# Optimization experiments

Hardware: AMD Instinct MI355X
Metric: run time of the kernel (lower is better)

## Reference

```python
import jax, jax.numpy as jnp
import numpy as np

NEG_INF = -1e30  # stand-in for -inf, safe under fp16/bf16 softmax masking via where below


def setup_inputs() -> dict:
    key = jax.random.key(0)
    ks = jax.random.split(key, 6)
    B, S, D, E = 4, 4096, 2048, 16
    x = jax.random.normal(ks[0], (B, S, D), dtype=jnp.float32)
    noise = jax.random.normal(ks[1], (B, S, E), dtype=jnp.float32)
    scale = 1.0 / np.sqrt(D)
    W_fc = jax.random.normal(ks[2], (E, D), dtype=jnp.float32) * scale
    b_fc = jnp.zeros((E,), dtype=jnp.float32)
    W_noisy = jax.random.normal(ks[3], (E, D), dtype=jnp.float32) * scale
    b_noisy = jnp.zeros((E,), dtype=jnp.float32)
    return {"x": x, "noise": noise, "W_fc": W_fc, "b_fc": b_fc,
            "W_noisy": W_noisy, "b_noisy": b_noisy}


def reference(x, noise, W_fc, b_fc, W_noisy, b_noisy):
    top_k = 2
    n_expert = W_fc.shape[0]
    # dual linear: [B,S,D] @ [D,E] -> [B,S,E]
    logits = jnp.einsum("bsd,ed->bse", x, W_fc) + b_fc
    noise_logits = jnp.einsum("bsd,ed->bse", x, W_noisy) + b_noisy
    noisy_logits = logits + noise * jax.nn.softplus(noise_logits)
    top_k_logits, ids = jax.lax.top_k(noisy_logits, top_k)  # [B,S,k]
    # scatter top-k values into a -inf-filled tensor == mask non-topk with -inf
    sel = jnp.any(jax.nn.one_hot(ids, n_expert, dtype=jnp.bool_), axis=-2)  # [B,S,E]
    sparse_logits = jnp.where(sel, noisy_logits, -jnp.inf)
    router_output = jax.nn.softmax(sparse_logits, axis=-1)
    return (router_output, ids)
```

## Files before the change

kernel.cpp:

```cpp
#include <hip/hip_runtime.h>
#include <hip/hip_bf16.h>

#define NROWS 16384
#define KD    2048
#define NE    16
#define ROWS_PER_BLK 64
#define KH    1024
#define TPH   16


__device__ __forceinline__ void gload_lds16(const float* g, float* l) {
    __builtin_amdgcn_global_load_lds(
        (const __attribute__((address_space(1))) void*)g,
        (__attribute__((address_space(3))) void*)l,
        16, 0, 0);
}

__global__ __launch_bounds__(512)
void noisy_router_kernel(const float* __restrict__ x,
                         const float* __restrict__ noise,
                         const float* __restrict__ Wfc,
                         const float* __restrict__ bfc,
                         const float* __restrict__ Wns,
                         const float* __restrict__ bns,
                         float* __restrict__ out)
{
    __shared__ float lds[32 * KH + ROWS_PER_BLK * 33];

    const int tid  = threadIdx.x;
    const int lane = tid & 63;
    const int w    = tid >> 6;
    const int eq   = w & 3;
    const int rh   = w >> 2;
    const int seg  = lane & 7;
    const int rgrp = lane >> 3;

    const int rowbase = blockIdx.x * ROWS_PER_BLK + rh * 32 + rgrp * 4;

    const int wrb  = tid >> 8;
    const int scol = (tid & 255) * 4;

    const float* xb = x + (size_t)rowbase * KD + seg * 8;

    float accA[4][4], accB[4][4];
    #pragma unroll
    for (int j = 0; j < 4; ++j)
        #pragma unroll
        for (int e = 0; e < 4; ++e) { accA[j][e] = 0.f; accB[j][e] = 0.f; }

    #pragma unroll 1
    for (int h = 0; h < 2; ++h) {
        const int kbase = h * KH;
        __syncthreads();
        {
            const float* srcF = Wfc + (size_t)wrb * KD + kbase + scol;
            const float* srcN = Wns + (size_t)wrb * KD + kbase + scol;
            #pragma unroll
            for (int i = 0; i < 8; ++i)
                gload_lds16(srcF + (size_t)(2 * i) * KD, lds + i * 2048 + tid * 4);
            #pragma unroll
            for (int i = 0; i < 8; ++i)
                gload_lds16(srcN + (size_t)(2 * i) * KD, lds + (8 + i) * 2048 + tid * 4);
        }
        __syncthreads();

        const float* wp0 = lds + (eq * 4) * KH + seg * 8;
        const float* wp1 = lds + (16 + eq * 4) * KH + seg * 8;
        const float* xh  = xb + kbase;

        #pragma unroll 2
        for (int t = 0; t < TPH; ++t) {
            float4 xv[4][2];
            #pragma unroll
            for (int j = 0; j < 4; ++j) {
                xv[j][0] = *(const float4*)(xh + (size_t)j * KD + t * 64);
                xv[j][1] = *(const float4*)(xh + (size_t)j * KD + t * 64 + 4);
            }
            #pragma unroll
            for (int e = 0; e < 4; ++e) {
                const float4 a0 = *(const float4*)(wp0 + e * KH + t * 64);
                const float4 a1 = *(const float4*)(wp0 + e * KH + t * 64 + 4);
                const float4 b0 = *(const float4*)(wp1 + e * KH + t * 64);
                const float4 b1 = *(const float4*)(wp1 + e * KH + t * 64 + 4);
                #pragma unroll
                for (int j = 0; j < 4; ++j) {
                    const float4 x0 = xv[j][0], x1 = xv[j][1];
                    float sA = accA[j][e], sB = accB[j][e];
                    sA = fmaf(x0.x, a0.x, sA); sA = fmaf(x0.y, a0.y, sA);
                    sA = fmaf(x0.z, a0.z, sA); sA = fmaf(x0.w, a0.w, sA);
                    sA = fmaf(x1.x, a1.x, sA); sA = fmaf(x1.y, a1.y, sA);
                    sA = fmaf(x1.z, a1.z, sA); sA = fmaf(x1.w, a1.w, sA);
                    sB = fmaf(x0.x, b0.x, sB); sB = fmaf(x0.y, b0.y, sB);
                    sB = fmaf(x0.z, b0.z, sB); sB = fmaf(x0.w, b0.w, sB);
                    sB = fmaf(x1.x, b1.x, sB); sB = fmaf(x1.y, b1.y, sB);
                    sB = fmaf(x1.z, b1.z, sB); sB = fmaf(x1.w, b1.w, sB);
                    accA[j][e] = sA; accB[j][e] = sB;
                }
            }
        }
    }

    #pragma unroll
    for (int j = 0; j < 4; ++j)
        #pragma unroll
        for (int e = 0; e < 4; ++e) {
            float a = accA[j][e], b = accB[j][e];
            a += __shfl_xor(a, 1); a += __shfl_xor(a, 2); a += __shfl_xor(a, 4);
            b += __shfl_xor(b, 1); b += __shfl_xor(b, 2); b += __shfl_xor(b, 4);
            accA[j][e] = a; accB[j][e] = b;
        }

    __syncthreads();
    float* const slab = lds + 32 * KH;

    if (seg == 0) {
        #pragma unroll
        for (int j = 0; j < 4; ++j) {
            float* dst = slab + (rh * 32 + rgrp * 4 + j) * 33 + eq * 4;
            #pragma unroll
            for (int e = 0; e < 4; ++e) { dst[e] = accA[j][e]; dst[16 + e] = accB[j][e]; }
        }
    }
    __syncthreads();

    if (tid < ROWS_PER_BLK) {
        const int r = tid;
        const float* rowp = slab + r * 33;
        const size_t grow = (size_t)blockIdx.x * ROWS_PER_BLK + r;
        const float* nzp = noise + grow * NE;

        float m1 = -1e30f, m2 = -1e30f;
        int i1 = 0, i2 = 0;
        #pragma unroll
        for (int j = 0; j < NE; ++j) {
            const float z  = rowp[16 + j] + bns[j];
            const float sp = fmaxf(z, 0.f) + log1pf(expf(-fabsf(z)));
            const float v  = fmaf(nzp[j], sp, rowp[j] + bfc[j]);
            if (v > m1)      { m2 = m1; i2 = i1; m1 = v; i1 = j; }
            else if (v > m2) { m2 = v;  i2 = j; }
        }
        const float e2  = expf(m2 - m1);
        const float inv = 1.f / (1.f + e2);

        float* po = out + grow * NE;
        #pragma unroll
        for (int j = 0; j < NE; ++j) {
            po[j] = (j == i1) ? inv : ((j == i2) ? e2 * inv : 0.f);
        }
        float* pi = out + (size_t)NROWS * NE + grow * 2;
        pi[0] = (float)i1;
        pi[1] = (float)i2;
    }
}

extern "C" void kernel_launch(void* const* d_in, const int* in_sizes, int n_in,
                              void* d_out, int out_size, void* d_ws, size_t ws_size,
                              hipStream_t stream)
{
    const float* x     = (const float*)d_in[0];
    const float* noise = (const float*)d_in[1];
    const float* Wfc   = (const float*)d_in[2];
    const float* bfc   = (const float*)d_in[3];
    const float* Wns   = (const float*)d_in[4];
    const float* bns   = (const float*)d_in[5];
    float* out = (float*)d_out;

    noisy_router_kernel<<<NROWS / ROWS_PER_BLK, 512, 0, stream>>>(
        x, noise, Wfc, bfc, Wns, bns, out);
}
```

Before: 48.66 us.

## Halve rows per block and split K across wave groups with LDS reduction

Reduces rows per block from 64 to 32, doubling the grid to 512 blocks. The two wave groups now split each K chunk rather than owning separate row halves. Weights are staged in four 512-wide phases instead of two 1024-wide ones, and the partial sums are combined through an LDS reduction. This aims to spread work across more CUs and cut LDS footprint for better occupancy, at the cost of twice the total weight staging traffic and an extra barrier and reduction step.

```diff
diff --git a/kernel.cpp b/kernel.cpp
--- a/kernel.cpp
+++ b/kernel.cpp
@@ -4,9 +4,10 @@
 #define NROWS 16384
 #define KD    2048
 #define NE    16
-#define ROWS_PER_BLK 64
-#define KH    1024
-#define TPH   16
+#define ROWS_PER_BLK 32
+#define KQ    512
+#define NPH   4
+#define TPP   8
 
 
 __device__ __forceinline__ void gload_lds16(const float* g, float* l) {
@@ -25,20 +26,20 @@
                          const float* __restrict__ bns,
                          float* __restrict__ out)
 {
-    __shared__ float lds[32 * KH + ROWS_PER_BLK * 33];
+    __shared__ float lds[32 * KQ + 2 * 32 * 33];
 
     const int tid  = threadIdx.x;
     const int lane = tid & 63;
     const int w    = tid >> 6;
     const int eq   = w & 3;
-    const int rh   = w >> 2;
+    const int kg   = w >> 2;
     const int seg  = lane & 7;
     const int rgrp = lane >> 3;
 
-    const int rowbase = blockIdx.x * ROWS_PER_BLK + rh * 32 + rgrp * 4;
+    const int rowbase = blockIdx.x * ROWS_PER_BLK + rgrp * 4;
 
-    const int wrb  = tid >> 8;
-    const int scol = (tid & 255) * 4;
+    const int swr  = tid >> 7;
+    const int scol = (tid & 127) * 4;
 
     const float* xb = x + (size_t)rowbase * KD + seg * 8;
 
@@ -49,27 +50,28 @@
         for (int e = 0; e < 4; ++e) { accA[j][e] = 0.f; accB[j][e] = 0.f; }
 
     #pragma unroll 1
-    for (int h = 0; h < 2; ++h) {
-        const int kbase = h * KH;
+    for (int p = 0; p < NPH; ++p) {
+        const int kbase = p * KQ;
         __syncthreads();
         {
-            const float* srcF = Wfc + (size_t)wrb * KD + kbase + scol;
-            const float* srcN = Wns + (size_t)wrb * KD + kbase + scol;
             #pragma unroll
-            for (int i = 0; i < 8; ++i)
-                gload_lds16(srcF + (size_t)(2 * i) * KD, lds + i * 2048 + tid * 4);
-            #pragma unroll
-            for (int i = 0; i < 8; ++i)
-                gload_lds16(srcN + (size_t)(2 * i) * KD, lds + (8 + i) * 2048 + tid * 4);
+            for (int i = 0; i < 8; ++i) {
+                const int wr = 4 * i + swr;
+                const float* gsrc = (wr < 16 ? Wfc + (size_t)wr * KD
+                                             : Wns + (size_t)(wr - 16) * KD)
+                                    + kbase + scol;
+                gload_lds16(gsrc, lds + i * 2048 + tid * 4);
+            }
         }
         __syncthreads();
 
-        const float* wp0 = lds + (eq * 4) * KH + seg * 8;
-        const float* wp1 = lds + (16 + eq * 4) * KH + seg * 8;
+        const float* wp0 = lds + (eq * 4) * KQ + seg * 8;
+        const float* wp1 = lds + (16 + eq * 4) * KQ + seg * 8;
         const float* xh  = xb + kbase;
 
         #pragma unroll 2
-        for (int t = 0; t < TPH; ++t) {
+        for (int c = 0; c < 4; ++c) {
+            const int t = kg * 4 + c;
             float4 xv[4][2];
             #pragma unroll
             for (int j = 0; j < 4; ++j) {
@@ -78,10 +80,10 @@
             }
             #pragma unroll
             for (int e = 0; e < 4; ++e) {
-                const float4 a0 = *(const float4*)(wp0 + e * KH + t * 64);
-                const float4 a1 = *(const float4*)(wp0 + e * KH + t * 64 + 4);
-                const float4 b0 = *(const float4*)(wp1 + e * KH + t * 64);
-                const float4 b1 = *(const float4*)(wp1 + e * KH + t * 64 + 4);
+                const float4 a0 = *(const float4*)(wp0 + e * KQ + t * 64);
+                const float4 a1 = *(const float4*)(wp0 + e * KQ + t * 64 + 4);
+                const float4 b0 = *(const float4*)(wp1 + e * KQ + t * 64);
+                const float4 b1 = *(const float4*)(wp1 + e * KQ + t * 64 + 4);
                 #pragma unroll
                 for (int j = 0; j < 4; ++j) {
                     const float4 x0 = xv[j][0], x1 = xv[j][1];
@@ -111,15 +113,24 @@
         }
 
     __syncthreads();
-    float* const slab = lds + 32 * KH;
+    float* const slab = lds + 32 * KQ;
 
     if (seg == 0) {
         #pragma unroll
         for (int j = 0; j < 4; ++j) {
-            float* dst = slab + (rh * 32 + rgrp * 4 + j) * 33 + eq * 4;
+            float* dst = slab + kg * 1056 + (rgrp * 4 + j) * 33 + eq * 4;
             #pragma unroll
             for (int e = 0; e < 4; ++e) { dst[e] = accA[j][e]; dst[16 + e] = accB[j][e]; }
         }
+    }
+    __syncthreads();
+
+    {
+        const int idx = tid * 2;
+        const int r   = idx >> 5;
+        const int o   = idx & 31;
+        slab[r * 33 + o]     += slab[1056 + r * 33 + o];
+        slab[r * 33 + o + 1] += slab[1056 + r * 33 + o + 1];
     }
     __syncthreads();
 
```

Measured after the change: 65.17 us. +33.9%, slower.

## Give each wave all 16 experts for 8 rows, drop LDS epilogue slab

Applied to the files above, without the earlier changes.

Changes the work split so each wave computes all 16 experts (both weight matrices) for 8 rows, instead of 4 experts across 32 rows. Each x row is now loaded once per block rather than by four waves, cutting redundant global x traffic. The epilogue no longer needs an LDS slab or extra barriers, because each row's full logits sit in the lanes that did the shuffle reduction. In exchange, per-thread register use (32 accumulators) and LDS weight reads per FMA go up, since weights are no longer reused across 4 rows in registers.

```diff
diff --git a/kernel.cpp b/kernel.cpp
--- a/kernel.cpp
+++ b/kernel.cpp
@@ -25,28 +25,24 @@
                          const float* __restrict__ bns,
                          float* __restrict__ out)
 {
-    __shared__ float lds[32 * KH + ROWS_PER_BLK * 33];
+    __shared__ float lds[32 * KH];
 
     const int tid  = threadIdx.x;
     const int lane = tid & 63;
     const int w    = tid >> 6;
-    const int eq   = w & 3;
-    const int rh   = w >> 2;
     const int seg  = lane & 7;
-    const int rgrp = lane >> 3;
+    const int rsub = lane >> 3;
 
-    const int rowbase = blockIdx.x * ROWS_PER_BLK + rh * 32 + rgrp * 4;
+    const int row = blockIdx.x * ROWS_PER_BLK + w * 8 + rsub;
 
     const int wrb  = tid >> 8;
     const int scol = (tid & 255) * 4;
 
-    const float* xb = x + (size_t)rowbase * KD + seg * 8;
+    const float* xr = x + (size_t)row * KD + seg * 8;
 
-    float accA[4][4], accB[4][4];
+    float accA[NE], accB[NE];
     #pragma unroll
-    for (int j = 0; j < 4; ++j)
-        #pragma unroll
-        for (int e = 0; e < 4; ++e) { accA[j][e] = 0.f; accB[j][e] = 0.f; }
+    for (int e = 0; e < NE; ++e) { accA[e] = 0.f; accB[e] = 0.f; }
 
     #pragma unroll 1
     for (int h = 0; h < 2; ++h) {
@@ -64,78 +60,53 @@
         }
         __syncthreads();
 
-        const float* wp0 = lds + (eq * 4) * KH + seg * 8;
-        const float* wp1 = lds + (16 + eq * 4) * KH + seg * 8;
-        const float* xh  = xb + kbase;
+        const float* wpF = lds + seg * 8;
+        const float* wpN = lds + 16 * KH + seg * 8;
+        const float* xh  = xr + kbase;
 
         #pragma unroll 2
         for (int t = 0; t < TPH; ++t) {
-            float4 xv[4][2];
+            const float4 x0 = *(const float4*)(xh + t * 64);
+            const float4 x1 = *(const float4*)(xh + t * 64 + 4);
             #pragma unroll
-            for (int j = 0; j < 4; ++j) {
-                xv[j][0] = *(const float4*)(xh + (size_t)j * KD + t * 64);
-                xv[j][1] = *(const float4*)(xh + (size_t)j * KD + t * 64 + 4);
-            }
-            #pragma unroll
-            for (int e = 0; e < 4; ++e) {
-                const float4 a0 = *(const float4*)(wp0 + e * KH + t * 64);
-                const float4 a1 = *(const float4*)(wp0 + e * KH + t * 64 + 4);
-                const float4 b0 = *(const float4*)(wp1 + e * KH + t * 64);
-                const float4 b1 = *(const float4*)(wp1 + e * KH + t * 64 + 4);
-                #pragma unroll
-                for (int j = 0; j < 4; ++j) {
-                    const float4 x0 = xv[j][0], x1 = xv[j][1];
-                    float sA = accA[j][e], sB = accB[j][e];
-                    sA = fmaf(x0.x, a0.x, sA); sA = fmaf(x0.y, a0.y, sA);
-                    sA = fmaf(x0.z, a0.z, sA); sA = fmaf(x0.w, a0.w, sA);
-                    sA = fmaf(x1.x, a1.x, sA); sA = fmaf(x1.y, a1.y, sA);
-                    sA = fmaf(x1.z, a1.z, sA); sA = fmaf(x1.w, a1.w, sA);
-                    sB = fmaf(x0.x, b0.x, sB); sB = fmaf(x0.y, b0.y, sB);
-                    sB = fmaf(x0.z, b0.z, sB); sB = fmaf(x0.w, b0.w, sB);
-                    sB = fmaf(x1.x, b1.x, sB); sB = fmaf(x1.y, b1.y, sB);
-                    sB = fmaf(x1.z, b1.z, sB); sB = fmaf(x1.w, b1.w, sB);
-                    accA[j][e] = sA; accB[j][e] = sB;
-                }
+            for (int e = 0; e < NE; ++e) {
+                const float4 a0 = *(const float4*)(wpF + e * KH + t * 64);
+                const float4 a1 = *(const float4*)(wpF + e * KH + t * 64 + 4);
+                const float4 b0 = *(const float4*)(wpN + e * KH + t * 64);
+                const float4 b1 = *(const float4*)(wpN + e * KH + t * 64 + 4);
+                float sA = accA[e], sB = accB[e];
+                sA = fmaf(x0.x, a0.x, sA); sA = fmaf(x0.y, a0.y, sA);
+                sA = fmaf(x0.z, a0.z, sA); sA = fmaf(x0.w, a0.w, sA);
+                sA = fmaf(x1.x, a1.x, sA); sA = fmaf(x1.y, a1.y, sA);
+                sA = fmaf(x1.z, a1.z, sA); sA = fmaf(x1.w, a1.w, sA);
+                sB = fmaf(x0.x, b0.x, sB); sB = fmaf(x0.y, b0.y, sB);
+                sB = fmaf(x0.z, b0.z, sB); sB = fmaf(x0.w, b0.w, sB);
+                sB = fmaf(x1.x, b1.x, sB); sB = fmaf(x1.y, b1.y, sB);
+                sB = fmaf(x1.z, b1.z, sB); sB = fmaf(x1.w, b1.w, sB);
+                accA[e] = sA; accB[e] = sB;
             }
         }
     }
 
     #pragma unroll
-    for (int j = 0; j < 4; ++j)
-        #pragma unroll
-        for (int e = 0; e < 4; ++e) {
-            float a = accA[j][e], b = accB[j][e];
-            a += __shfl_xor(a, 1); a += __shfl_xor(a, 2); a += __shfl_xor(a, 4);
-            b += __shfl_xor(b, 1); b += __shfl_xor(b, 2); b += __shfl_xor(b, 4);
-            accA[j][e] = a; accB[j][e] = b;
-        }
-
-    __syncthreads();
-    float* const slab = lds + 32 * KH;
+    for (int e = 0; e < NE; ++e) {
+        float a = accA[e], b = accB[e];
+        a += __shfl_xor(a, 1); a += __shfl_xor(a, 2); a += __shfl_xor(a, 4);
+        b += __shfl_xor(b, 1); b += __shfl_xor(b, 2); b += __shfl_xor(b, 4);
+        accA[e] = a; accB[e] = b;
+    }
 
     if (seg == 0) {
-        #pragma unroll
-        for (int j = 0; j < 4; ++j) {
-            float* dst = slab + (rh * 32 + rgrp * 4 + j) * 33 + eq * 4;
-            #pragma unroll
-            for (int e = 0; e < 4; ++e) { dst[e] = accA[j][e]; dst[16 + e] = accB[j][e]; }
-        }
-    }
-    __syncthreads();
-
-    if (tid < ROWS_PER_BLK) {
-        const int r = tid;
-        const float* rowp = slab + r * 33;
-        const size_t grow = (size_t)blockIdx.x * ROWS_PER_BLK + r;
+        const size_t grow = (size_t)row;
         const float* nzp = noise + grow * NE;
 
         float m1 = -1e30f, m2 = -1e30f;
         int i1 = 0, i2 = 0;
         #pragma unroll
         for (int j = 0; j < NE; ++j) {
-            const float z  = rowp[16 + j] + bns[j];
+            const float z  = accB[j] + bns[j];
             const float sp = fmaxf(z, 0.f) + log1pf(expf(-fabsf(z)));
-            const float v  = fmaf(nzp[j], sp, rowp[j] + bfc[j]);
+            const float v  = fmaf(nzp[j], sp, accA[j] + bfc[j]);
             if (v > m1)      { m2 = m1; i2 = i1; m1 = v; i1 = j; }
             else if (v > m2) { m2 = v;  i2 = j; }
         }
```

Measured after the change: 81.48 us. 1.67x slower.
